# Performance work log

Measured on AMD Instinct MI355X. Metric: run time of the kernel, lower is better.

## Reference

```python
import jax, jax.numpy as jnp
import numpy as np

B, L, D = 2, 2048, 1024
H = 16
HD = D // H  # 64
WINDOW = 256


def setup_inputs() -> dict:
    key = jax.random.key(0)
    k1, k2, k3 = jax.random.split(key, 3)
    s = 0.02
    return {
        "x": jax.random.normal(k1, (B, L, D), dtype=jnp.float32),
        "w_qkv": jax.random.normal(k2, (D, 3 * D), dtype=jnp.float32) * s,
        "b_qkv": jnp.zeros((3 * D,), dtype=jnp.float32),
        "w_out": jax.random.normal(k3, (D, D), dtype=jnp.float32) * s,
        "b_out": jnp.zeros((D,), dtype=jnp.float32),
    }


def _window_mask(seq_len, window_size, dtype):
    # row i allows cols in [i - w//2, i + w//2] inclusive (symmetric band)
    half = window_size // 2
    i = jnp.arange(seq_len)[:, None]
    j = jnp.arange(seq_len)[None, :]
    allowed = jnp.abs(i - j) <= half
    return jnp.where(allowed, jnp.zeros((), dtype), jnp.asarray(-jnp.inf, dtype))


def reference(x, w_qkv, b_qkv, w_out, b_out):
    b, l, d = x.shape
    qkv = x @ w_qkv + b_qkv                        # [B, L, 3D]
    qkv = qkv.reshape(b, l, 3, H, HD)
    q = jnp.transpose(qkv[:, :, 0], (0, 2, 1, 3))   # [B, H, L, HD]
    k = jnp.transpose(qkv[:, :, 1], (0, 2, 1, 3))
    v = jnp.transpose(qkv[:, :, 2], (0, 2, 1, 3))
    scale = 1.0 / np.sqrt(HD)
    scores = jnp.einsum("bhqd,bhkd->bhqk", q, k) * scale
    scores = scores + _window_mask(l, WINDOW, scores.dtype)[None, None]
    attn = jax.nn.softmax(scores, axis=-1)          # dropout: eval mode (p applied only in training)
    out = jnp.einsum("bhqk,bhkd->bhqd", attn, v)    # [B, H, L, HD]
    out = jnp.transpose(out, (0, 2, 1, 3)).reshape(b, l, d)
    return out @ w_out + b_out
```

## Files before the change

### kernel.cpp

```cpp
#include <hip/hip_runtime.h>
#include <math.h>

#define B_    2
#define L_    2048
#define D_    1024
#define H_    16
#define HD_   64
#define HALF_ 128

typedef __attribute__((ext_vector_type(8))) short short8;
typedef __attribute__((ext_vector_type(4))) float f32x4;

__device__ __forceinline__ unsigned short f2bf(float x) {
  unsigned int u = __float_as_uint(x);
  u = (u + 0x7fffu + ((u >> 16) & 1u)) >> 16;
  return (unsigned short)u;
}

__device__ __forceinline__ void async_cp16(const unsigned short* g, unsigned short* l) {
  __builtin_amdgcn_global_load_lds(
      (const __attribute__((address_space(1))) unsigned int*)g,
      (__attribute__((address_space(3))) unsigned int*)l, 16, 0, 0);
}

__device__ __forceinline__ void tr_round32(const float* __restrict__ in,
                                           unsigned short* __restrict__ hi,
                                           int N, int K, int n0, int k0,
                                           float (*t)[33], int tid) {
  {
    const int kl = tid >> 3, nl = (tid & 7) * 4;
    const float4 v = *(const float4*)&in[(size_t)(k0 + kl) * N + n0 + nl];
    t[kl][nl + 0] = v.x; t[kl][nl + 1] = v.y;
    t[kl][nl + 2] = v.z; t[kl][nl + 3] = v.w;
  }
  __syncthreads();
  {
    const int no = tid >> 3, ko = (tid & 7) * 4;
    ushort4 h;
    h.x = f2bf(t[ko + 0][no]);
    h.y = f2bf(t[ko + 1][no]);
    h.z = f2bf(t[ko + 2][no]);
    h.w = f2bf(t[ko + 3][no]);
    *(ushort4*)&hi[(size_t)(n0 + no) * K + k0 + ko] = h;
  }
}

__global__ __launch_bounds__(256) void prep(const float* __restrict__ x,
                                            unsigned short* __restrict__ x_hi,
                                            const float* __restrict__ w_qkv,
                                            unsigned short* __restrict__ wqkvT,
                                            const float* __restrict__ w_out,
                                            unsigned short* __restrict__ woutT) {
  __shared__ float t[32][33];
  const int bx = blockIdx.x, tid = threadIdx.x;
  if (bx < 4096) {
    const int i = (bx * 256 + tid) * 4;
    const float4 a = *(const float4*)&x[i];
    ushort4 h;
    h.x = f2bf(a.x); h.y = f2bf(a.y); h.z = f2bf(a.z); h.w = f2bf(a.w);
    *(ushort4*)&x_hi[i] = h;
  } else if (bx < 7168) {
    const int tb = bx - 4096;
    tr_round32(w_qkv, wqkvT, 3 * D_, D_, (tb % 96) * 32, (tb / 96) * 32, t, tid);
  } else {
    const int tb = bx - 7168;
    tr_round32(w_out, woutT, D_, D_, (tb % 32) * 32, (tb / 32) * 32, t, tid);
  }
}

__global__ __launch_bounds__(256, 3) void gemm_qkv(
    const unsigned short* __restrict__ Ah,
    const unsigned short* __restrict__ Bh,
    const float* __restrict__ bias,
    unsigned short* __restrict__ q_hi,
    unsigned short* __restrict__ kT,
    unsigned short* __restrict__ vTile,
    int N, int K) {
  __shared__ char smraw[33792];
  const int tid  = threadIdx.x;
  const int wave = tid >> 6, lane = tid & 63;

  const int lin = blockIdx.y * gridDim.x + blockIdx.x;
  const int swz = (lin & 7) * 96 + (lin >> 3);
  const int n0 = (swz % 24) * 128, m0 = (swz / 24) * 128;

  const int wm = (wave >> 1) * 64, wn = (wave & 1) * 64;
  const int quad = lane >> 4, ln16 = lane & 15;

  const bool isA = wave < 2;
  const unsigned short* src = isA ? Ah : Bh;
  const int baserow = isA ? m0 : n0;
  const int instbase = (wave & 1) * 8;
  const int dbase = (isA ? 0 : 16384) + instbase * 1024;
  size_t goff[8];
#pragma unroll
  for (int i = 0; i < 8; ++i) {
    const int r = (instbase + i) * 8 + (lane >> 3);
    const int c = (lane & 7) ^ (r & 7);
    goff[i] = (size_t)(baserow + r) * K + c * 8;
  }

  int offA[4], offB[4];
#pragma unroll
  for (int t = 0; t < 4; ++t) {
    const int r = wm + t * 16 + ln16;
    offA[t] = r * 128 + ((quad ^ (r & 7)) * 16);
    const int rn = wn + t * 16 + ln16;
    offB[t] = 16384 + rn * 128 + ((quad ^ (rn & 7)) * 16);
  }

  f32x4 acc[4][4] = {};
  const char* smb = (const char*)smraw;

  for (int k0 = 0; k0 < K; k0 += 64) {
#pragma unroll
    for (int i = 0; i < 8; ++i)
      async_cp16(src + goff[i] + k0,
                 (unsigned short*)(smraw + dbase + i * 1024));
    __syncthreads();

    {
      short8 ah[4], bh[4];
#pragma unroll
      for (int t = 0; t < 4; ++t) {
        ah[t] = *(const short8*)(smb + offA[t]);
        bh[t] = *(const short8*)(smb + offB[t]);
      }
#pragma unroll
      for (int t = 0; t < 4; ++t)
#pragma unroll
        for (int u = 0; u < 4; ++u)
          acc[t][u] = __builtin_amdgcn_mfma_f32_16x16x32_bf16(bh[u], ah[t], acc[t][u], 0, 0, 0);
    }
    {
      short8 ah[4], bh[4];
#pragma unroll
      for (int t = 0; t < 4; ++t) {
        ah[t] = *(const short8*)(smb + (offA[t] ^ 64));
        bh[t] = *(const short8*)(smb + (offB[t] ^ 64));
      }
#pragma unroll
      for (int t = 0; t < 4; ++t)
#pragma unroll
        for (int u = 0; u < 4; ++u)
          acc[t][u] = __builtin_amdgcn_mfma_f32_16x16x32_bf16(bh[u], ah[t], acc[t][u], 0, 0, 0);
    }
    __syncthreads();
  }

  const int slot = n0 >> 10;
  const int nbase = n0 & 1023;

  if (slot == 0) {
#pragma unroll
    for (int t = 0; t < 4; ++t) {
      const int m = m0 + wm + t * 16 + ln16;
#pragma unroll
      for (int u = 0; u < 4; ++u) {
        const int nl = wn + u * 16 + quad * 4;
        const float4 bq = *(const float4*)&bias[n0 + nl];
        ushort4 h;
        h.x = f2bf(acc[t][u][0] + bq.x);
        h.y = f2bf(acc[t][u][1] + bq.y);
        h.z = f2bf(acc[t][u][2] + bq.z);
        h.w = f2bf(acc[t][u][3] + bq.w);
        *(ushort4*)&q_hi[(size_t)m * 1024 + nbase + nl] = h;
      }
    }
  } else if (slot == 1) {
#pragma unroll
    for (int t = 0; t < 4; ++t) {
      const int tok = m0 + wm + t * 16 + ln16;
      const int bb = tok >> 11, j = tok & 2047;
#pragma unroll
      for (int u = 0; u < 4; ++u) {
        const int nl = wn + u * 16 + quad * 4;
        const float4 bq = *(const float4*)&bias[n0 + nl];
        const int hd = nbase + nl;
        const int hh_ = hd >> 6, dg = (hd & 63) >> 3, di = hd & 7;
        ushort4 h;
        h.x = f2bf(acc[t][u][0] + bq.x);
        h.y = f2bf(acc[t][u][1] + bq.y);
        h.z = f2bf(acc[t][u][2] + bq.z);
        h.w = f2bf(acc[t][u][3] + bq.w);
        const size_t o =
            ((((size_t)bb * 16 + hh_) * 8 + dg) * 2048 + j) * 8 + di;
        *(ushort4*)&kT[o] = h;
      }
    }
  } else {
    unsigned short* lt = (unsigned short*)smraw;
#pragma unroll
    for (int t = 0; t < 4; ++t) {
      const int ml = wm + t * 16 + ln16;
#pragma unroll
      for (int u = 0; u < 4; ++u) {
        const int nl = wn + u * 16 + quad * 4;
        const float4 bq = *(const float4*)&bias[n0 + nl];
        ushort4 h;
        h.x = f2bf(acc[t][u][0] + bq.x);
        h.y = f2bf(acc[t][u][1] + bq.y);
        h.z = f2bf(acc[t][u][2] + bq.z);
        h.w = f2bf(acc[t][u][3] + bq.w);
        *(ushort4*)&lt[ml * 132 + nl] = h;
      }
    }
    __syncthreads();
    const int jg0 = (m0 & 2047) >> 3;
    const int bb = m0 >> 11;
#pragma unroll
    for (int it = 0; it < 8; ++it) {
      const int chunk = it * 256 + tid;
      const int hd = chunk & 127, tokg = chunk >> 7;
      short8 hh;
#pragma unroll
      for (int s = 0; s < 8; ++s)
        hh[s] = (short)lt[(tokg * 8 + s) * 132 + hd];
      const size_t o =
          (((size_t)bb * 256 + jg0 + tokg) * 1024 + nbase + hd) * 8;
      *(short8*)&vTile[o] = hh;
    }
  }
}

__global__ __launch_bounds__(256, 2) void gemm_out(
    const unsigned short* __restrict__ Ah,
    const unsigned short* __restrict__ Bh,
    const float* __restrict__ bias,
    float* __restrict__ C,
    int N, int K) {
  __shared__ char smraw[24576];
  const int tid  = threadIdx.x;
  const int wave = tid >> 6, lane = tid & 63;

  const int lin = blockIdx.y * gridDim.x + blockIdx.x;
  const int swz = (lin & 7) * 64 + (lin >> 3);
  const int n0 = (swz % 16) * 64, m0 = (swz / 16) * 128;

  const int quad = lane >> 4, ln16 = lane & 15;
  const int wm = wave * 32;

  const unsigned short* sptr[6];
  int dstoff[6];
#pragma unroll
  for (int s = 0; s < 6; ++s) {
    const int g = wave * 6 + s;
    const bool isA = g < 16;
    const unsigned short* base = isA ? Ah : Bh;
    const int r0 = isA ? g * 8 : (g - 16) * 8;
    const int r = r0 + (lane >> 3);
    const int c = (lane & 7) ^ (r & 7);
    sptr[s] = base + (size_t)((isA ? m0 : n0) + r) * K + c * 8;
    dstoff[s] = isA ? g * 1024 : 16384 + (g - 16) * 1024;
  }

  int offA[2], offB[4];
#pragma unroll
  for (int t = 0; t < 2; ++t) {
    const int r = wm + t * 16 + ln16;
    offA[t] = r * 128 + ((quad ^ (r & 7)) * 16);
  }
#pragma unroll
  for (int u = 0; u < 4; ++u) {
    const int rn = u * 16 + ln16;
    offB[u] = 16384 + rn * 128 + ((quad ^ (rn & 7)) * 16);
  }

  f32x4 acc[2][4] = {};
  const char* smb = (const char*)smraw;

  for (int k0 = 0; k0 < K; k0 += 64) {
#pragma unroll
    for (int s = 0; s < 6; ++s)
      async_cp16(sptr[s] + k0, (unsigned short*)(smraw + dstoff[s]));
    __syncthreads();

    {
      short8 ah[2], bh[4];
#pragma unroll
      for (int t = 0; t < 2; ++t) ah[t] = *(const short8*)(smb + offA[t]);
#pragma unroll
      for (int u = 0; u < 4; ++u) bh[u] = *(const short8*)(smb + offB[u]);
#pragma unroll
      for (int t = 0; t < 2; ++t)
#pragma unroll
        for (int u = 0; u < 4; ++u)
          acc[t][u] = __builtin_amdgcn_mfma_f32_16x16x32_bf16(bh[u], ah[t], acc[t][u], 0, 0, 0);
    }
    {
      short8 ah[2], bh[4];
#pragma unroll
      for (int t = 0; t < 2; ++t) ah[t] = *(const short8*)(smb + (offA[t] ^ 64));
#pragma unroll
      for (int u = 0; u < 4; ++u) bh[u] = *(const short8*)(smb + (offB[u] ^ 64));
#pragma unroll
      for (int t = 0; t < 2; ++t)
#pragma unroll
        for (int u = 0; u < 4; ++u)
          acc[t][u] = __builtin_amdgcn_mfma_f32_16x16x32_bf16(bh[u], ah[t], acc[t][u], 0, 0, 0);
    }
    __syncthreads();
  }

#pragma unroll
  for (int t = 0; t < 2; ++t) {
    const int m = m0 + wm + t * 16 + ln16;
#pragma unroll
    for (int u = 0; u < 4; ++u) {
      const int n = n0 + u * 16 + quad * 4;
      const float4 bq = *(const float4*)&bias[n];
      float4 o;
      o.x = acc[t][u][0] + bq.x;
      o.y = acc[t][u][1] + bq.y;
      o.z = acc[t][u][2] + bq.z;
      o.w = acc[t][u][3] + bq.w;
      *(float4*)&C[(size_t)m * N + n] = o;
    }
  }
}

__global__ __launch_bounds__(256) void attn_mfma(
    const unsigned short* __restrict__ q_hi,
    const unsigned short* __restrict__ kT,
    const unsigned short* __restrict__ vTile,
    unsigned short* __restrict__ attn_h) {
  __shared__ float ob[64 * 68];

  const int b   = blockIdx.z;
  const int h   = blockIdx.y;
  const int i0  = blockIdx.x * 64;
  const int tid = threadIdx.x;
  const int mt  = tid >> 6, lane = tid & 63;
  const int quad = lane >> 4, ln16 = lane & 15;
  const int jlo = i0 - HALF_;

  const size_t qbase =
      (size_t)(b * L_ + i0 + mt * 16 + ln16) * 1024 + h * 64 + quad * 8;
  const short8 qh0 = *(const short8*)&q_hi[qbase];
  const short8 qh1 = *(const short8*)&q_hi[qbase + 32];

  const size_t kb0 = (((size_t)b * 16 + h) * 8 + quad) * 2048 * 8;
  const size_t kb1 = (((size_t)b * 16 + h) * 8 + quad + 4) * 2048 * 8;

  const int iabs = i0 + mt * 16 + ln16;

  f32x4 o[4] = {};
  float s = 0.f;

#pragma unroll
  for (int c = 0; c < 10; ++c) {
    const int base = jlo + c * 32;

    const int j0c = min(max(base + ln16, 0), L_ - 1);
    const int j1c = min(max(base + 16 + ln16, 0), L_ - 1);
    const short8 k00 = *(const short8*)&kT[kb0 + (size_t)j0c * 8];
    const short8 k01 = *(const short8*)&kT[kb1 + (size_t)j0c * 8];
    const short8 k10 = *(const short8*)&kT[kb0 + (size_t)j1c * 8];
    const short8 k11 = *(const short8*)&kT[kb1 + (size_t)j1c * 8];

    const int jv = min(max(base + quad * 8, 0), L_ - 8);
    const size_t vgb = ((size_t)b * 256 + (jv >> 3)) * 1024 + h * 64;
    short8 vh[4];
#pragma unroll
    for (int t = 0; t < 4; ++t)
      vh[t] = *(const short8*)&vTile[(vgb + t * 16 + ln16) * 8];

    f32x4 a0 = {}, a1 = {};
    a0 = __builtin_amdgcn_mfma_f32_16x16x32_bf16(k00, qh0, a0, 0, 0, 0);
    a0 = __builtin_amdgcn_mfma_f32_16x16x32_bf16(k01, qh1, a0, 0, 0, 0);
    a1 = __builtin_amdgcn_mfma_f32_16x16x32_bf16(k10, qh0, a1, 0, 0, 0);
    a1 = __builtin_amdgcn_mfma_f32_16x16x32_bf16(k11, qh1, a1, 0, 0, 0);

    unsigned int pk00, pk01, pk10, pk11;
    {
      float ev[4];
#pragma unroll
      for (int e = 0; e < 4; ++e) {
        const int jabs = base + quad * 4 + e;
        const bool ok = (jabs >= 0) && (jabs < L_) && (abs(iabs - jabs) <= HALF_);
        ev[e] = ok ? __expf(a0[e] * 0.125f) : 0.f;
        s += ev[e];
      }
      pk00 = (unsigned)f2bf(ev[0]) | ((unsigned)f2bf(ev[1]) << 16);
      pk01 = (unsigned)f2bf(ev[2]) | ((unsigned)f2bf(ev[3]) << 16);
    }
    {
      float ev[4];
#pragma unroll
      for (int e = 0; e < 4; ++e) {
        const int jabs = base + 16 + quad * 4 + e;
        const bool ok = (jabs >= 0) && (jabs < L_) && (abs(iabs - jabs) <= HALF_);
        ev[e] = ok ? __expf(a1[e] * 0.125f) : 0.f;
        s += ev[e];
      }
      pk10 = (unsigned)f2bf(ev[0]) | ((unsigned)f2bf(ev[1]) << 16);
      pk11 = (unsigned)f2bf(ev[2]) | ((unsigned)f2bf(ev[3]) << 16);
    }

    const int src0 = ((quad & 1) * 2) * 16 + ln16;
    const int src1 = src0 + 16;
    const unsigned a0w = (unsigned)__shfl((int)pk00, src0);
    const unsigned b0w = (unsigned)__shfl((int)pk10, src0);
    const unsigned a1w = (unsigned)__shfl((int)pk01, src0);
    const unsigned b1w = (unsigned)__shfl((int)pk11, src0);
    const unsigned a2w = (unsigned)__shfl((int)pk00, src1);
    const unsigned b2w = (unsigned)__shfl((int)pk10, src1);
    const unsigned a3w = (unsigned)__shfl((int)pk01, src1);
    const unsigned b3w = (unsigned)__shfl((int)pk11, src1);
    int4 wv;
    wv.x = (int)((quad < 2) ? a0w : b0w);
    wv.y = (int)((quad < 2) ? a1w : b1w);
    wv.z = (int)((quad < 2) ? a2w : b2w);
    wv.w = (int)((quad < 2) ? a3w : b3w);
    const short8 pf = *(const short8*)&wv;

#pragma unroll
    for (int t = 0; t < 4; ++t)
      o[t] = __builtin_amdgcn_mfma_f32_16x16x32_bf16(pf, vh[t], o[t], 0, 0, 0);
  }

  s += __shfl_xor(s, 16);
  s += __shfl_xor(s, 32);
  float rinv[4];
#pragma unroll
  for (int e = 0; e < 4; ++e)
    rinv[e] = 1.f / __shfl(s, quad * 4 + e);

#pragma unroll
  for (int t = 0; t < 4; ++t)
#pragma unroll
    for (int e = 0; e < 4; ++e)
      ob[(mt * 16 + quad * 4 + e) * 68 + t * 16 + ln16] = o[t][e] * rinv[e];
  __syncthreads();
#pragma unroll
  for (int pass = 0; pass < 2; ++pass) {
    const int rr = pass * 32 + (tid >> 3), ck = tid & 7;
    const float* rp = &ob[rr * 68 + ck * 8];
    const float4 f0 = *(const float4*)&rp[0];
    const float4 f1 = *(const float4*)&rp[4];
    short8 hh;
    hh[0] = (short)f2bf(f0.x); hh[1] = (short)f2bf(f0.y);
    hh[2] = (short)f2bf(f0.z); hh[3] = (short)f2bf(f0.w);
    hh[4] = (short)f2bf(f1.x); hh[5] = (short)f2bf(f1.y);
    hh[6] = (short)f2bf(f1.z); hh[7] = (short)f2bf(f1.w);
    const size_t oo = ((size_t)(b * L_ + i0 + rr)) * 1024 + h * 64 + ck * 8;
    *(short8*)&attn_h[oo] = hh;
  }
}

extern "C" void kernel_launch(void* const* d_in, const int* in_sizes, int n_in,
                              void* d_out, int out_size, void* d_ws, size_t ws_size,
                              hipStream_t stream) {
  const float* x     = (const float*)d_in[0];
  const float* w_qkv = (const float*)d_in[1];
  const float* b_qkv = (const float*)d_in[2];
  const float* w_out = (const float*)d_in[3];
  const float* b_out = (const float*)d_in[4];
  float* out = (float*)d_out;

  const int M = B_ * L_;

  char* ws = (char*)d_ws;
  unsigned short* x_hi    = (unsigned short*)(ws + 0);
  unsigned short* wqkvT   = (unsigned short*)(ws + 16777216);
  unsigned short* woutT   = (unsigned short*)(ws + 23068672);
  unsigned short* q_hi    = (unsigned short*)(ws + 25165824);
  unsigned short* kT      = (unsigned short*)(ws + 33554432);
  unsigned short* vTile   = (unsigned short*)(ws + 41943040);
  unsigned short* attn_hi = (unsigned short*)(ws + 0);

  prep<<<8192, 256, 0, stream>>>(x, x_hi, w_qkv, wqkvT, w_out, woutT);
  {
    dim3 g(3072 / 128, M / 128);
    gemm_qkv<<<g, 256, 0, stream>>>(x_hi, wqkvT, b_qkv, q_hi, kT, vTile,
                                    3072, D_);
  }
  {
    dim3 g(L_ / 64, H_, B_);
    attn_mfma<<<g, 256, 0, stream>>>(q_hi, kT, vTile, attn_hi);
  }
  {
    dim3 g(D_ / 64, M / 128);
    gemm_out<<<g, 256, 0, stream>>>(attn_hi, woutT, b_out, out, D_, D_);
  }
}
```

Baseline: 157.4 us.

## Triple-buffer K=32 async LDS loads in QKV and output GEMMs

Both GEMM main loops now use a three-stage ring of LDS buffers with K-step 32. Async global-to-LDS copies are issued two stages ahead, and a partial vmcnt wait plus a single barrier per iteration replaces the old load, sync, compute, sync pattern. The LDS layout is reswizzled for 64-byte rows. This is meant to hide global load latency behind MFMA work, at the cost of more LDS per block (48KB and 36KB), which may lower occupancy. K is hard-coded to 1024 (32 iterations).

```diff
diff --git a/kernel.cpp b/kernel.cpp
--- a/kernel.cpp
+++ b/kernel.cpp
@@ -76,7 +76,7 @@
     unsigned short* __restrict__ kT,
     unsigned short* __restrict__ vTile,
     int N, int K) {
-  __shared__ char smraw[33792];
+  __shared__ char smraw[49152];
   const int tid  = threadIdx.x;
   const int wave = tid >> 6, lane = tid & 63;
 
@@ -87,65 +87,73 @@
   const int wm = (wave >> 1) * 64, wn = (wave & 1) * 64;
   const int quad = lane >> 4, ln16 = lane & 15;
 
-  const bool isA = wave < 2;
-  const unsigned short* src = isA ? Ah : Bh;
-  const int baserow = isA ? m0 : n0;
-  const int instbase = (wave & 1) * 8;
-  const int dbase = (isA ? 0 : 16384) + instbase * 1024;
-  size_t goff[8];
-#pragma unroll
-  for (int i = 0; i < 8; ++i) {
-    const int r = (instbase + i) * 8 + (lane >> 3);
-    const int c = (lane & 7) ^ (r & 7);
-    goff[i] = (size_t)(baserow + r) * K + c * 8;
-  }
-
+  const int srow   = lane >> 2;
+  const int schunk = (lane & 3) ^ ((lane >> 3) & 3);
+  size_t ga[2], gb[2];
+  int dA[2], dB[2];
+#pragma unroll
+  for (int i = 0; i < 2; ++i) {
+    const int r = i * 64 + wave * 16 + srow;
+    ga[i] = (size_t)(m0 + r) * K + schunk * 8;
+    gb[i] = (size_t)(n0 + r) * K + schunk * 8;
+    dA[i] = i * 4096 + wave * 1024;
+    dB[i] = 8192 + i * 4096 + wave * 1024;
+  }
+
+  const int sterm = ((ln16 >> 1) & 3);
   int offA[4], offB[4];
 #pragma unroll
   for (int t = 0; t < 4; ++t) {
-    const int r = wm + t * 16 + ln16;
-    offA[t] = r * 128 + ((quad ^ (r & 7)) * 16);
+    const int r  = wm + t * 16 + ln16;
+    offA[t] = r * 64 + ((quad ^ sterm) * 16);
     const int rn = wn + t * 16 + ln16;
-    offB[t] = 16384 + rn * 128 + ((quad ^ (rn & 7)) * 16);
+    offB[t] = 8192 + rn * 64 + ((quad ^ sterm) * 16);
   }
 
   f32x4 acc[4][4] = {};
-  const char* smb = (const char*)smraw;
-
-  for (int k0 = 0; k0 < K; k0 += 64) {
-#pragma unroll
-    for (int i = 0; i < 8; ++i)
-      async_cp16(src + goff[i] + k0,
-                 (unsigned short*)(smraw + dbase + i * 1024));
-    __syncthreads();
-
-    {
-      short8 ah[4], bh[4];
-#pragma unroll
-      for (int t = 0; t < 4; ++t) {
-        ah[t] = *(const short8*)(smb + offA[t]);
-        bh[t] = *(const short8*)(smb + offB[t]);
+
+  {
+    char* b0 = smraw;
+    char* b1 = smraw + 16384;
+#pragma unroll
+    for (int i = 0; i < 2; ++i) {
+      async_cp16(Ah + ga[i], (unsigned short*)(b0 + dA[i]));
+      async_cp16(Bh + gb[i], (unsigned short*)(b0 + dB[i]));
+    }
+#pragma unroll
+    for (int i = 0; i < 2; ++i) {
+      async_cp16(Ah + ga[i] + 32, (unsigned short*)(b1 + dA[i]));
+      async_cp16(Bh + gb[i] + 32, (unsigned short*)(b1 + dB[i]));
+    }
+  }
+  asm volatile("s_waitcnt vmcnt(4)" ::: "memory");
+  __builtin_amdgcn_s_barrier();
+
+  for (int kt = 0; kt < 32; ++kt) {
+    if (kt < 30) {
+      char* bs = smraw + ((kt + 2) % 3) * 16384;
+      const int ko = (kt + 2) * 32;
+#pragma unroll
+      for (int i = 0; i < 2; ++i) {
+        async_cp16(Ah + ga[i] + ko, (unsigned short*)(bs + dA[i]));
+        async_cp16(Bh + gb[i] + ko, (unsigned short*)(bs + dB[i]));
       }
-#pragma unroll
-      for (int t = 0; t < 4; ++t)
-#pragma unroll
-        for (int u = 0; u < 4; ++u)
-          acc[t][u] = __builtin_amdgcn_mfma_f32_16x16x32_bf16(bh[u], ah[t], acc[t][u], 0, 0, 0);
-    }
-    {
-      short8 ah[4], bh[4];
-#pragma unroll
-      for (int t = 0; t < 4; ++t) {
-        ah[t] = *(const short8*)(smb + (offA[t] ^ 64));
-        bh[t] = *(const short8*)(smb + (offB[t] ^ 64));
-      }
-#pragma unroll
-      for (int t = 0; t < 4; ++t)
-#pragma unroll
-        for (int u = 0; u < 4; ++u)
-          acc[t][u] = __builtin_amdgcn_mfma_f32_16x16x32_bf16(bh[u], ah[t], acc[t][u], 0, 0, 0);
-    }
-    __syncthreads();
+    }
+    const char* buf = smraw + (kt % 3) * 16384;
+    short8 ah[4], bh[4];
+#pragma unroll
+    for (int t = 0; t < 4; ++t) {
+      ah[t] = *(const short8*)(buf + offA[t]);
+      bh[t] = *(const short8*)(buf + offB[t]);
+    }
+#pragma unroll
+    for (int t = 0; t < 4; ++t)
+#pragma unroll
+      for (int u = 0; u < 4; ++u)
+        acc[t][u] = __builtin_amdgcn_mfma_f32_16x16x32_bf16(bh[u], ah[t], acc[t][u], 0, 0, 0);
+    if (kt < 30) asm volatile("s_waitcnt vmcnt(4)" ::: "memory");
+    else         asm volatile("s_waitcnt vmcnt(0)" ::: "memory");
+    __builtin_amdgcn_s_barrier();
   }
 
   const int slot = n0 >> 10;
@@ -229,7 +237,7 @@
     const float* __restrict__ bias,
     float* __restrict__ C,
     int N, int K) {
-  __shared__ char smraw[24576];
+  __shared__ char smraw[36864];
   const int tid  = threadIdx.x;
   const int wave = tid >> 6, lane = tid & 63;
 
@@ -240,66 +248,72 @@
   const int quad = lane >> 4, ln16 = lane & 15;
   const int wm = wave * 32;
 
-  const unsigned short* sptr[6];
-  int dstoff[6];
-#pragma unroll
-  for (int s = 0; s < 6; ++s) {
-    const int g = wave * 6 + s;
-    const bool isA = g < 16;
-    const unsigned short* base = isA ? Ah : Bh;
-    const int r0 = isA ? g * 8 : (g - 16) * 8;
-    const int r = r0 + (lane >> 3);
-    const int c = (lane & 7) ^ (r & 7);
-    sptr[s] = base + (size_t)((isA ? m0 : n0) + r) * K + c * 8;
-    dstoff[s] = isA ? g * 1024 : 16384 + (g - 16) * 1024;
-  }
-
+  const int srow   = lane >> 2;
+  const int schunk = (lane & 3) ^ ((lane >> 3) & 3);
+  size_t ga[2], gbo;
+  int dA[2], dBo;
+#pragma unroll
+  for (int i = 0; i < 2; ++i) {
+    const int r = i * 64 + wave * 16 + srow;
+    ga[i] = (size_t)(m0 + r) * K + schunk * 8;
+    dA[i] = i * 4096 + wave * 1024;
+  }
+  {
+    const int r = wave * 16 + srow;
+    gbo = (size_t)(n0 + r) * K + schunk * 8;
+    dBo = 8192 + wave * 1024;
+  }
+
+  const int sterm = ((ln16 >> 1) & 3);
   int offA[2], offB[4];
 #pragma unroll
   for (int t = 0; t < 2; ++t) {
     const int r = wm + t * 16 + ln16;
-    offA[t] = r * 128 + ((quad ^ (r & 7)) * 16);
+    offA[t] = r * 64 + ((quad ^ sterm) * 16);
   }
 #pragma unroll
   for (int u = 0; u < 4; ++u) {
     const int rn = u * 16 + ln16;
-    offB[u] = 16384 + rn * 128 + ((quad ^ (rn & 7)) * 16);
+    offB[u] = 8192 + rn * 64 + ((quad ^ sterm) * 16);
   }
 
   f32x4 acc[2][4] = {};
-  const char* smb = (const char*)smraw;
-
-  for (int k0 = 0; k0 < K; k0 += 64) {
-#pragma unroll
-    for (int s = 0; s < 6; ++s)
-      async_cp16(sptr[s] + k0, (unsigned short*)(smraw + dstoff[s]));
-    __syncthreads();
-
-    {
-      short8 ah[2], bh[4];
-#pragma unroll
-      for (int t = 0; t < 2; ++t) ah[t] = *(const short8*)(smb + offA[t]);
-#pragma unroll
-      for (int u = 0; u < 4; ++u) bh[u] = *(const short8*)(smb + offB[u]);
-#pragma unroll
-      for (int t = 0; t < 2; ++t)
-#pragma unroll
-        for (int u = 0; u < 4; ++u)
-          acc[t][u] = __builtin_amdgcn_mfma_f32_16x16x32_bf16(bh[u], ah[t], acc[t][u], 0, 0, 0);
-    }
-    {
-      short8 ah[2], bh[4];
-#pragma unroll
-      for (int t = 0; t < 2; ++t) ah[t] = *(const short8*)(smb + (offA[t] ^ 64));
-#pragma unroll
-      for (int u = 0; u < 4; ++u) bh[u] = *(const short8*)(smb + (offB[u] ^ 64));
-#pragma unroll
-      for (int t = 0; t < 2; ++t)
-#pragma unroll
-        for (int u = 0; u < 4; ++u)
-          acc[t][u] = __builtin_amdgcn_mfma_f32_16x16x32_bf16(bh[u], ah[t], acc[t][u], 0, 0, 0);
-    }
-    __syncthreads();
+
+#pragma unroll
+  for (int kt = 0; kt < 2; ++kt) {
+    char* bs = smraw + kt * 12288;
+    const int ko = kt * 32;
+#pragma unroll
+    for (int i = 0; i < 2; ++i)
+      async_cp16(Ah + ga[i] + ko, (unsigned short*)(bs + dA[i]));
+    async_cp16(Bh + gbo + ko, (unsigned short*)(bs + dBo));
+  }
+  asm volatile("s_waitcnt vmcnt(3)" ::: "memory");
+  __builtin_amdgcn_s_barrier();
+
+  for (int kt = 0; kt < 32; ++kt) {
+    if (kt < 30) {
+      char* bs = smraw + ((kt + 2) % 3) * 12288;
+      const int ko = (kt + 2) * 32;
+#pragma unroll
+      for (int i = 0; i < 2; ++i)
+        async_cp16(Ah + ga[i] + ko, (unsigned short*)(bs + dA[i]));
+      async_cp16(Bh + gbo + ko, (unsigned short*)(bs + dBo));
+    }
+    const char* buf = smraw + (kt % 3) * 12288;
+    short8 ah[2], bh[4];
+#pragma unroll
+    for (int t = 0; t < 2; ++t) ah[t] = *(const short8*)(buf + offA[t]);
+#pragma unroll
+    for (int u = 0; u < 4; ++u) bh[u] = *(const short8*)(buf + offB[u]);
+#pragma unroll
+    for (int t = 0; t < 2; ++t)
+#pragma unroll
+      for (int u = 0; u < 4; ++u)
+        acc[t][u] = __builtin_amdgcn_mfma_f32_16x16x32_bf16(bh[u], ah[t], acc[t][u], 0, 0, 0);
+    if (kt < 30) asm volatile("s_waitcnt vmcnt(3)" ::: "memory");
+    else         asm volatile("s_waitcnt vmcnt(0)" ::: "memory");
+    __builtin_amdgcn_s_barrier();
   }
 
 #pragma unroll
```

Result: no change. 160.3 us (+1.9%).

## Prefetch K/V fragments one chunk ahead, remap blocks per XCD, raise MFMA priority

Applied to the files above, without the earlier changes.

The attention kernel now loads the next chunk's K and V fragments into a second register set while it computes on the current chunk, which hides global load latency. It also remaps the linear block index so each XCD handles a contiguous set of (batch, head) pairs, aimed at better L2 reuse of K/V. s_setprio is raised around the MFMA groups. The cost is more register pressure from the doubled fragment buffers, which may lower occupancy. The remap assumes grid dimensions of 32x16x2.

```diff
diff --git a/kernel.cpp b/kernel.cpp
--- a/kernel.cpp
+++ b/kernel.cpp
@@ -326,13 +326,16 @@
     unsigned short* __restrict__ attn_h) {
   __shared__ float ob[64 * 68];
 
-  const int b   = blockIdx.z;
-  const int h   = blockIdx.y;
-  const int i0  = blockIdx.x * 64;
   const int tid = threadIdx.x;
   const int mt  = tid >> 6, lane = tid & 63;
   const int quad = lane >> 4, ln16 = lane & 15;
-  const int jlo = i0 - HALF_;
+
+  const int lin  = blockIdx.x + gridDim.x * (blockIdx.y + gridDim.y * blockIdx.z);
+  const int xcd  = lin & 7, idx = lin >> 3;
+  const int pair = xcd * 4 + (idx >> 5);
+  const int i0   = (idx & 31) * 64;
+  const int b    = pair >> 4, h = pair & 15;
+  const int jlo  = i0 - HALF_;
 
   const size_t qbase =
       (size_t)(b * L_ + i0 + mt * 16 + ln16) * 1024 + h * 64 + quad * 8;
@@ -347,29 +350,50 @@
   f32x4 o[4] = {};
   float s = 0.f;
 
-#pragma unroll
-  for (int c = 0; c < 10; ++c) {
-    const int base = jlo + c * 32;
-
+  short8 kf[2][4], vf[2][4];
+  {
+    const int base = jlo;
     const int j0c = min(max(base + ln16, 0), L_ - 1);
     const int j1c = min(max(base + 16 + ln16, 0), L_ - 1);
-    const short8 k00 = *(const short8*)&kT[kb0 + (size_t)j0c * 8];
-    const short8 k01 = *(const short8*)&kT[kb1 + (size_t)j0c * 8];
-    const short8 k10 = *(const short8*)&kT[kb0 + (size_t)j1c * 8];
-    const short8 k11 = *(const short8*)&kT[kb1 + (size_t)j1c * 8];
-
+    kf[0][0] = *(const short8*)&kT[kb0 + (size_t)j0c * 8];
+    kf[0][1] = *(const short8*)&kT[kb1 + (size_t)j0c * 8];
+    kf[0][2] = *(const short8*)&kT[kb0 + (size_t)j1c * 8];
+    kf[0][3] = *(const short8*)&kT[kb1 + (size_t)j1c * 8];
     const int jv = min(max(base + quad * 8, 0), L_ - 8);
     const size_t vgb = ((size_t)b * 256 + (jv >> 3)) * 1024 + h * 64;
-    short8 vh[4];
 #pragma unroll
     for (int t = 0; t < 4; ++t)
-      vh[t] = *(const short8*)&vTile[(vgb + t * 16 + ln16) * 8];
+      vf[0][t] = *(const short8*)&vTile[(vgb + t * 16 + ln16) * 8];
+  }
+
+#pragma unroll
+  for (int c = 0; c < 10; ++c) {
+    const int cur = c & 1, nxt = cur ^ 1;
+
+    if (c < 9) {
+      const int nb = jlo + (c + 1) * 32;
+      const int j0c = min(max(nb + ln16, 0), L_ - 1);
+      const int j1c = min(max(nb + 16 + ln16, 0), L_ - 1);
+      kf[nxt][0] = *(const short8*)&kT[kb0 + (size_t)j0c * 8];
+      kf[nxt][1] = *(const short8*)&kT[kb1 + (size_t)j0c * 8];
+      kf[nxt][2] = *(const short8*)&kT[kb0 + (size_t)j1c * 8];
+      kf[nxt][3] = *(const short8*)&kT[kb1 + (size_t)j1c * 8];
+      const int jv = min(max(nb + quad * 8, 0), L_ - 8);
+      const size_t vgb = ((size_t)b * 256 + (jv >> 3)) * 1024 + h * 64;
+#pragma unroll
+      for (int t = 0; t < 4; ++t)
+        vf[nxt][t] = *(const short8*)&vTile[(vgb + t * 16 + ln16) * 8];
+    }
+
+    const int base = jlo + c * 32;
 
     f32x4 a0 = {}, a1 = {};
-    a0 = __builtin_amdgcn_mfma_f32_16x16x32_bf16(k00, qh0, a0, 0, 0, 0);
-    a0 = __builtin_amdgcn_mfma_f32_16x16x32_bf16(k01, qh1, a0, 0, 0, 0);
-    a1 = __builtin_amdgcn_mfma_f32_16x16x32_bf16(k10, qh0, a1, 0, 0, 0);
-    a1 = __builtin_amdgcn_mfma_f32_16x16x32_bf16(k11, qh1, a1, 0, 0, 0);
+    __builtin_amdgcn_s_setprio(1);
+    a0 = __builtin_amdgcn_mfma_f32_16x16x32_bf16(kf[cur][0], qh0, a0, 0, 0, 0);
+    a0 = __builtin_amdgcn_mfma_f32_16x16x32_bf16(kf[cur][1], qh1, a0, 0, 0, 0);
+    a1 = __builtin_amdgcn_mfma_f32_16x16x32_bf16(kf[cur][2], qh0, a1, 0, 0, 0);
+    a1 = __builtin_amdgcn_mfma_f32_16x16x32_bf16(kf[cur][3], qh1, a1, 0, 0, 0);
+    __builtin_amdgcn_s_setprio(0);
 
     unsigned int pk00, pk01, pk10, pk11;
     {
@@ -414,9 +438,11 @@
     wv.w = (int)((quad < 2) ? a3w : b3w);
     const short8 pf = *(const short8*)&wv;
 
+    __builtin_amdgcn_s_setprio(1);
 #pragma unroll
     for (int t = 0; t < 4; ++t)
-      o[t] = __builtin_amdgcn_mfma_f32_16x16x32_bf16(pf, vh[t], o[t], 0, 0, 0);
+      o[t] = __builtin_amdgcn_mfma_f32_16x16x32_bf16(pf, vf[cur][t], o[t], 0, 0, 0);
+    __builtin_amdgcn_s_setprio(0);
   }
 
   s += __shfl_xor(s, 16);
```

After: 155.9 us (median of 2 runs). No clear change (-0.9%).
